# Kernel tuning notes

Hardware: AMD Instinct MI355X
Metric: run time of the kernel (lower is better)

The kernel has to match this reference:

```python
import jax, jax.numpy as jnp
import numpy as np

N, E, IN_DIM, OUT_DIM, SEM_DIM = 50000, 800000, 128, 128, 128
EPS = 1e-8


def setup_inputs() -> dict:
    key = jax.random.key(0)
    k = jax.random.split(key, 8)
    x = jax.random.normal(k[0], (N, IN_DIM), dtype=jnp.float32)
    edge_index = jax.random.randint(k[1], (2, E), 0, N, dtype=jnp.int64)
    semantic_vec = jax.random.normal(k[2], (N, SEM_DIM), dtype=jnp.float32)
    s = 1.0 / np.sqrt(IN_DIM)
    W_src = jax.random.uniform(k[3], (OUT_DIM, IN_DIM), jnp.float32, -s, s)
    b_src = jax.random.uniform(k[4], (OUT_DIM,), jnp.float32, -s, s)
    W_dst = jax.random.uniform(k[5], (OUT_DIM, IN_DIM), jnp.float32, -s, s)
    b_dst = jax.random.uniform(k[6], (OUT_DIM,), jnp.float32, -s, s)
    return {"x": x, "edge_index": edge_index, "semantic_vec": semantic_vec,
            "W_src": W_src, "b_src": b_src, "W_dst": W_dst, "b_dst": b_dst}


def _scatter_softmax(sim, dst, num_segments):
    # numerically stable segment-wise softmax over edges grouped by dst
    seg_max = jax.ops.segment_max(sim, dst, num_segments=num_segments)
    seg_max = jnp.where(jnp.isneginf(seg_max), 0.0, seg_max)
    e = jnp.exp(sim - seg_max[dst])
    seg_sum = jax.ops.segment_sum(e, dst, num_segments=num_segments)
    return e / (seg_sum[dst] + 1e-16)


def reference(x, edge_index, semantic_vec, W_src, b_src, W_dst, b_dst):
    src, dst = edge_index[0], edge_index[1]
    x_j = x[src] @ W_src.T + b_src           # [E, out_dim]
    # cosine similarity with torch eps semantics
    a = semantic_vec[src]
    b = semantic_vec[dst]
    na = jnp.maximum(jnp.linalg.norm(a, axis=-1), EPS)
    nb = jnp.maximum(jnp.linalg.norm(b, axis=-1), EPS)
    sim = jnp.sum(a * b, axis=-1) / (na * nb)  # [E]
    attn = _scatter_softmax(sim, dst, x.shape[0])
    msg = attn[:, None] * x_j                 # [E, out_dim]
    out = jax.ops.segment_sum(msg, dst, num_segments=x.shape[0])
    return out
```

## Files before the change

### kernel.cpp

```cpp
#include <hip/hip_runtime.h>
#include <hip/hip_fp16.h>

#define Nn 50000
#define Ee 800000
#define D  128
#define SLOT 64

#define B_GEMM 782
#define B_SLOT 3125
#define B_NORM 12500

struct h4 { __half2 lo, hi; };

typedef _Float16 f16x8 __attribute__((ext_vector_type(8)));
typedef float    f32x4 __attribute__((ext_vector_type(4)));

__global__ __launch_bounds__(256) void k_prep(const float* __restrict__ x,
                                              const float* __restrict__ W,
                                              const float* __restrict__ b,
                                              const int* __restrict__ ei,
                                              const float* __restrict__ sem,
                                              __half* __restrict__ y16,
                                              __half* __restrict__ sem16,
                                              int* __restrict__ cnt,
                                              int* __restrict__ slotS) {
  __shared__ __half sW[128 * 136] __attribute__((aligned(16)));
  int bid = blockIdx.x, tid = threadIdx.x;

  if (bid < B_GEMM) {
    for (int i = tid; i < 128 * 32; i += 256) {
      int r = i >> 5, c4 = (i & 31) << 2;
      float4 w = *(const float4*)(W + (size_t)r * 128 + c4);
      __half2* dst = (__half2*)&sW[r * 136 + c4];
      dst[0] = __floats2half2_rn(w.x, w.y);
      dst[1] = __floats2half2_rn(w.z, w.w);
    }
    __syncthreads();

    int wave = tid >> 6, lane = tid & 63;
    int g = lane >> 4;
    int n16 = lane & 15;
    int m0 = bid * 64 + wave * 16;
    int mA = m0 + n16; if (mA > Nn - 1) mA = Nn - 1;
    const float4* xr = (const float4*)(x + (size_t)mA * 128);

    f32x4 acc[8];
#pragma unroll
    for (int jt = 0; jt < 8; jt++) {
      float bias = b[jt * 16 + n16];
      acc[jt] = (f32x4){bias, bias, bias, bias};
    }

#pragma unroll
    for (int kt = 0; kt < 4; kt++) {
      float4 xa = xr[kt * 8 + g * 2];
      float4 xb = xr[kt * 8 + g * 2 + 1];
      f16x8 a;
      a[0] = (_Float16)xa.x; a[1] = (_Float16)xa.y; a[2] = (_Float16)xa.z; a[3] = (_Float16)xa.w;
      a[4] = (_Float16)xb.x; a[5] = (_Float16)xb.y; a[6] = (_Float16)xb.z; a[7] = (_Float16)xb.w;
#pragma unroll
      for (int jt = 0; jt < 8; jt++) {
        f16x8 bf = *(const f16x8*)(&sW[(jt * 16 + n16) * 136 + kt * 32 + g * 8]);
        acc[jt] = __builtin_amdgcn_mfma_f32_16x16x32_f16(a, bf, acc[jt], 0, 0, 0);
      }
    }

#pragma unroll
    for (int jt = 0; jt < 8; jt++) {
#pragma unroll
      for (int r = 0; r < 4; r++) {
        int row = m0 + g * 4 + r;
        if (row < Nn)
          y16[(size_t)row * 128 + jt * 16 + n16] = __float2half(acc[jt][r]);
      }
    }
  } else if (bid < B_GEMM + B_SLOT) {
    int e = (bid - B_GEMM) * 256 + tid;
    if (e < Ee) {
      int s = ei[e], d = ei[Ee + e];
      int pos = atomicAdd(cnt + d, 1);
      if (pos < SLOT)
        slotS[(size_t)d * SLOT + pos] = s;
    }
  } else {
    int n = ((bid - B_GEMM - B_SLOT) * 256 + tid) >> 6;
    int lane = tid & 63;
    if (n < Nn) {
      const float2 v = *(const float2*)(sem + (size_t)n * D + 2 * lane);
      float p = v.x * v.x + v.y * v.y;
#pragma unroll
      for (int off = 32; off > 0; off >>= 1) p += __shfl_xor(p, off);
      float inv = 1.0f / fmaxf(sqrtf(p), 1e-8f);
      *(__half2*)(sem16 + (size_t)n * D + 2 * lane) = __floats2half2_rn(v.x * inv, v.y * inv);
    }
  }
}

__global__ __launch_bounds__(256) void k_fused(const __half* __restrict__ sem16,
                                               const __half* __restrict__ y16,
                                               const int* __restrict__ slotS,
                                               const int* __restrict__ cnt,
                                               float* __restrict__ out) {
  int d = (blockIdx.x * 256 + threadIdx.x) >> 6;
  int lane = threadIdx.x & 63;
  if (d >= Nn) return;
  int sub = lane >> 5, l32 = lane & 31;
  int c = cnt[d]; if (c > SLOT) c = SLOT;

  int sv = 0;
  if (lane < c) sv = slotS[(size_t)d * SLOT + lane];

  h4 dref = ((const h4*)(sem16 + (size_t)d * D))[l32];
  float2 d0 = __half22float2(dref.lo), d1 = __half22float2(dref.hi);

  float ev = 0.0f;
  for (int i = 0; i < c; i += 4) {
    int ia = i + sub, ib = i + 2 + sub;
    int sa = __shfl(sv, ia < c ? ia : c - 1);
    int sb = __shfl(sv, ib < c ? ib : c - 1);
    h4 ra = ((const h4*)(sem16 + (size_t)sa * D))[l32];
    h4 rb = ((const h4*)(sem16 + (size_t)sb * D))[l32];
    float2 ra0 = __half22float2(ra.lo), ra1 = __half22float2(ra.hi);
    float2 rb0 = __half22float2(rb.lo), rb1 = __half22float2(rb.hi);
    float pa = d0.x * ra0.x + d0.y * ra0.y + d1.x * ra1.x + d1.y * ra1.y;
    float pb = d0.x * rb0.x + d0.y * rb0.y + d1.x * rb1.x + d1.y * rb1.y;
#pragma unroll
    for (int o = 16; o > 0; o >>= 1) { pa += __shfl_xor(pa, o); pb += __shfl_xor(pb, o); }
    float ea = expf(pa), eb = expf(pb);
    float va = __shfl(ea, (lane - i) << 5);
    float vb = __shfl(eb, (lane - i - 2) << 5);
    if (lane >= i     && lane < i + 2 && lane < c) ev = va;
    if (lane >= i + 2 && lane < i + 4 && lane < c) ev = vb;
  }

  float S = ev;
#pragma unroll
  for (int o = 32; o > 0; o >>= 1) S += __shfl_xor(S, o);
  float inv = 1.0f / (S + 1e-16f);

  float o0 = 0, o1 = 0, o2 = 0, o3 = 0;
  for (int i = 0; i < c; i += 4) {
    int ia = i + sub, ib = i + 2 + sub;
    int ca = ia < c ? ia : c - 1, cb = ib < c ? ib : c - 1;
    int sa = __shfl(sv, ca), sb = __shfl(sv, cb);
    float wa_r = __shfl(ev, ca), wb_r = __shfl(ev, cb);
    float wa = (ia < c) ? wa_r : 0.0f;
    float wb = (ib < c) ? wb_r : 0.0f;
    h4 ya = ((const h4*)(y16 + (size_t)sa * D))[l32];
    h4 yb = ((const h4*)(y16 + (size_t)sb * D))[l32];
    float2 ya0 = __half22float2(ya.lo), ya1 = __half22float2(ya.hi);
    float2 yb0 = __half22float2(yb.lo), yb1 = __half22float2(yb.hi);
    o0 += wa * ya0.x + wb * yb0.x;
    o1 += wa * ya0.y + wb * yb0.y;
    o2 += wa * ya1.x + wb * yb1.x;
    o3 += wa * ya1.y + wb * yb1.y;
  }
  o0 += __shfl_xor(o0, 32); o1 += __shfl_xor(o1, 32);
  o2 += __shfl_xor(o2, 32); o3 += __shfl_xor(o3, 32);
  if (sub == 0) {
    float4 r; r.x = o0 * inv; r.y = o1 * inv; r.z = o2 * inv; r.w = o3 * inv;
    *(float4*)(out + (size_t)d * D + l32 * 4) = r;
  }
}

extern "C" void kernel_launch(void* const* d_in, const int* in_sizes, int n_in,
                              void* d_out, int out_size, void* d_ws, size_t ws_size,
                              hipStream_t stream) {
  const float* x     = (const float*)d_in[0];
  const int*   ei    = (const int*)d_in[1];
  const float* sem   = (const float*)d_in[2];
  const float* W_src = (const float*)d_in[3];
  const float* b_src = (const float*)d_in[4];
  float* out = (float*)d_out;

  char* ws = (char*)d_ws;
  const size_t O_Y    = 0;
  const size_t O_S16  = 12800000;
  const size_t O_CNT  = 25600000;
  const size_t O_SS   = 25800000;
  const size_t NEED   = 38600000;
  if (ws_size < NEED) return;

  __half* y16   = (__half*)(ws + O_Y);
  __half* sem16 = (__half*)(ws + O_S16);
  int* cnt   = (int*)(ws + O_CNT);
  int* slotS = (int*)(ws + O_SS);

  hipMemsetAsync(cnt, 0, Nn * sizeof(int), stream);
  k_prep<<<B_GEMM + B_SLOT + B_NORM, 256, 0, stream>>>(x, W_src, b_src, ei, sem,
                                                       y16, sem16, cnt, slotS);
  k_fused<<<(Nn + 3) / 4, 256, 0, stream>>>(sem16, y16, slotS, cnt, out);
}
```

Before: 228.5 us.

## Widen per-iteration gathers, use fdot2, drop LDS weight staging, coarsen prep blocks

The fused kernel now handles four neighbors per half-wave per iteration instead of two, computes the cosine dot with packed fp16 dot instructions, and stores exp values in shared memory instead of shuffling them. Normalization is folded into the weights before aggregation. In the prep kernel, the GEMM reads W directly from global/L2 and converts it in registers instead of staging fp16 W in LDS, and the scatter and norm blocks each process more items per thread. These aim to raise memory-level parallelism and cut block and LDS overhead, at the cost of redundant W loads per wave and more register pressure.

```diff
diff --git a/kernel.cpp b/kernel.cpp
--- a/kernel.cpp
+++ b/kernel.cpp
@@ -7,13 +7,30 @@
 #define SLOT 64
 
 #define B_GEMM 782
-#define B_SLOT 3125
-#define B_NORM 12500
+#define B_SCAT 1563
+#define B_NORM 3125
 
 struct h4 { __half2 lo, hi; };
 
 typedef _Float16 f16x8 __attribute__((ext_vector_type(8)));
+typedef _Float16 f16x2 __attribute__((ext_vector_type(2)));
 typedef float    f32x4 __attribute__((ext_vector_type(4)));
+
+union H2 { __half2 h; f16x2 v; };
+
+__device__ __forceinline__ float dot4(h4 a, h4 b, float acc) {
+#if __has_builtin(__builtin_amdgcn_fdot2)
+  H2 al, ah, bl, bh;
+  al.h = a.lo; ah.h = a.hi; bl.h = b.lo; bh.h = b.hi;
+  acc = __builtin_amdgcn_fdot2(al.v, bl.v, acc, false);
+  acc = __builtin_amdgcn_fdot2(ah.v, bh.v, acc, false);
+  return acc;
+#else
+  float2 a0 = __half22float2(a.lo), a1 = __half22float2(a.hi);
+  float2 b0 = __half22float2(b.lo), b1 = __half22float2(b.hi);
+  return acc + a0.x * b0.x + a0.y * b0.y + a1.x * b1.x + a1.y * b1.y;
+#endif
+}
 
 __global__ __launch_bounds__(256) void k_prep(const float* __restrict__ x,
                                               const float* __restrict__ W,
@@ -24,19 +41,9 @@
                                               __half* __restrict__ sem16,
                                               int* __restrict__ cnt,
                                               int* __restrict__ slotS) {
-  __shared__ __half sW[128 * 136] __attribute__((aligned(16)));
   int bid = blockIdx.x, tid = threadIdx.x;
 
   if (bid < B_GEMM) {
-    for (int i = tid; i < 128 * 32; i += 256) {
-      int r = i >> 5, c4 = (i & 31) << 2;
-      float4 w = *(const float4*)(W + (size_t)r * 128 + c4);
-      __half2* dst = (__half2*)&sW[r * 136 + c4];
-      dst[0] = __floats2half2_rn(w.x, w.y);
-      dst[1] = __floats2half2_rn(w.z, w.w);
-    }
-    __syncthreads();
-
     int wave = tid >> 6, lane = tid & 63;
     int g = lane >> 4;
     int n16 = lane & 15;
@@ -60,7 +67,11 @@
       a[4] = (_Float16)xb.x; a[5] = (_Float16)xb.y; a[6] = (_Float16)xb.z; a[7] = (_Float16)xb.w;
 #pragma unroll
       for (int jt = 0; jt < 8; jt++) {
-        f16x8 bf = *(const f16x8*)(&sW[(jt * 16 + n16) * 136 + kt * 32 + g * 8]);
+        const float4* wr = (const float4*)(W + (size_t)(jt * 16 + n16) * 128 + kt * 32 + g * 8);
+        float4 w0 = wr[0], w1 = wr[1];
+        f16x8 bf;
+        bf[0] = (_Float16)w0.x; bf[1] = (_Float16)w0.y; bf[2] = (_Float16)w0.z; bf[3] = (_Float16)w0.w;
+        bf[4] = (_Float16)w1.x; bf[5] = (_Float16)w1.y; bf[6] = (_Float16)w1.z; bf[7] = (_Float16)w1.w;
         acc[jt] = __builtin_amdgcn_mfma_f32_16x16x32_f16(a, bf, acc[jt], 0, 0, 0);
       }
     }
@@ -74,18 +85,24 @@
           y16[(size_t)row * 128 + jt * 16 + n16] = __float2half(acc[jt][r]);
       }
     }
-  } else if (bid < B_GEMM + B_SLOT) {
-    int e = (bid - B_GEMM) * 256 + tid;
-    if (e < Ee) {
-      int s = ei[e], d = ei[Ee + e];
-      int pos = atomicAdd(cnt + d, 1);
-      if (pos < SLOT)
-        slotS[(size_t)d * SLOT + pos] = s;
+  } else if (bid < B_GEMM + B_SCAT) {
+    int base = (bid - B_GEMM) * 512 + tid;
+#pragma unroll
+    for (int u = 0; u < 2; u++) {
+      int e = base + u * 256;
+      if (e < Ee) {
+        int s = ei[e], d = ei[Ee + e];
+        int pos = atomicAdd(cnt + d, 1);
+        if (pos < SLOT)
+          slotS[(size_t)d * SLOT + pos] = s;
+      }
     }
   } else {
-    int n = ((bid - B_GEMM - B_SLOT) * 256 + tid) >> 6;
-    int lane = tid & 63;
-    if (n < Nn) {
+    int nb = (bid - B_GEMM - B_SCAT) * 16;
+    int wave = tid >> 6, lane = tid & 63;
+#pragma unroll
+    for (int it = 0; it < 4; it++) {
+      int n = nb + it * 4 + wave;
       const float2 v = *(const float2*)(sem + (size_t)n * D + 2 * lane);
       float p = v.x * v.x + v.y * v.y;
 #pragma unroll
@@ -101,64 +118,79 @@
                                                const int* __restrict__ slotS,
                                                const int* __restrict__ cnt,
                                                float* __restrict__ out) {
-  int d = (blockIdx.x * 256 + threadIdx.x) >> 6;
-  int lane = threadIdx.x & 63;
+  __shared__ float sev[4][SLOT];
+  int w = threadIdx.x >> 6, lane = threadIdx.x & 63;
+  int d = blockIdx.x * 4 + w;
   if (d >= Nn) return;
   int sub = lane >> 5, l32 = lane & 31;
   int c = cnt[d]; if (c > SLOT) c = SLOT;
 
-  int sv = 0;
-  if (lane < c) sv = slotS[(size_t)d * SLOT + lane];
+  int sv = (lane < c) ? slotS[(size_t)d * SLOT + lane] : 0;
 
   h4 dref = ((const h4*)(sem16 + (size_t)d * D))[l32];
-  float2 d0 = __half22float2(dref.lo), d1 = __half22float2(dref.hi);
-
-  float ev = 0.0f;
-  for (int i = 0; i < c; i += 4) {
-    int ia = i + sub, ib = i + 2 + sub;
-    int sa = __shfl(sv, ia < c ? ia : c - 1);
-    int sb = __shfl(sv, ib < c ? ib : c - 1);
-    h4 ra = ((const h4*)(sem16 + (size_t)sa * D))[l32];
-    h4 rb = ((const h4*)(sem16 + (size_t)sb * D))[l32];
-    float2 ra0 = __half22float2(ra.lo), ra1 = __half22float2(ra.hi);
-    float2 rb0 = __half22float2(rb.lo), rb1 = __half22float2(rb.hi);
-    float pa = d0.x * ra0.x + d0.y * ra0.y + d1.x * ra1.x + d1.y * ra1.y;
-    float pb = d0.x * rb0.x + d0.y * rb0.y + d1.x * rb1.x + d1.y * rb1.y;
-#pragma unroll
-    for (int o = 16; o > 0; o >>= 1) { pa += __shfl_xor(pa, o); pb += __shfl_xor(pb, o); }
-    float ea = expf(pa), eb = expf(pb);
-    float va = __shfl(ea, (lane - i) << 5);
-    float vb = __shfl(eb, (lane - i - 2) << 5);
-    if (lane >= i     && lane < i + 2 && lane < c) ev = va;
-    if (lane >= i + 2 && lane < i + 4 && lane < c) ev = vb;
-  }
-
+
+  for (int i = 0; i < c; i += 8) {
+    float p0 = 0, p1 = 0, p2 = 0, p3 = 0;
+    int i0 = i + sub * 4;
+    int c0 = min(i0,     c - 1), c1 = min(i0 + 1, c - 1);
+    int c2 = min(i0 + 2, c - 1), c3 = min(i0 + 3, c - 1);
+    int s0 = __shfl(sv, c0), s1 = __shfl(sv, c1);
+    int s2 = __shfl(sv, c2), s3 = __shfl(sv, c3);
+    h4 r0 = ((const h4*)(sem16 + (size_t)s0 * D))[l32];
+    h4 r1 = ((const h4*)(sem16 + (size_t)s1 * D))[l32];
+    h4 r2 = ((const h4*)(sem16 + (size_t)s2 * D))[l32];
+    h4 r3 = ((const h4*)(sem16 + (size_t)s3 * D))[l32];
+    p0 = dot4(dref, r0, p0); p1 = dot4(dref, r1, p1);
+    p2 = dot4(dref, r2, p2); p3 = dot4(dref, r3, p3);
+#pragma unroll
+    for (int o = 16; o > 0; o >>= 1) {
+      p0 += __shfl_xor(p0, o); p1 += __shfl_xor(p1, o);
+      p2 += __shfl_xor(p2, o); p3 += __shfl_xor(p3, o);
+    }
+    float pe = p0;
+    pe = (l32 == 1) ? p1 : pe;
+    pe = (l32 == 2) ? p2 : pe;
+    pe = (l32 == 3) ? p3 : pe;
+    int iu = i0 + l32;
+    if (l32 < 4 && iu < c) sev[w][iu] = __expf(pe);
+  }
+
+  float ev = (lane < c) ? sev[w][lane] : 0.0f;
   float S = ev;
 #pragma unroll
   for (int o = 32; o > 0; o >>= 1) S += __shfl_xor(S, o);
-  float inv = 1.0f / (S + 1e-16f);
+  float evs = ev / (S + 1e-16f);
 
   float o0 = 0, o1 = 0, o2 = 0, o3 = 0;
-  for (int i = 0; i < c; i += 4) {
-    int ia = i + sub, ib = i + 2 + sub;
-    int ca = ia < c ? ia : c - 1, cb = ib < c ? ib : c - 1;
-    int sa = __shfl(sv, ca), sb = __shfl(sv, cb);
-    float wa_r = __shfl(ev, ca), wb_r = __shfl(ev, cb);
-    float wa = (ia < c) ? wa_r : 0.0f;
-    float wb = (ib < c) ? wb_r : 0.0f;
-    h4 ya = ((const h4*)(y16 + (size_t)sa * D))[l32];
-    h4 yb = ((const h4*)(y16 + (size_t)sb * D))[l32];
-    float2 ya0 = __half22float2(ya.lo), ya1 = __half22float2(ya.hi);
-    float2 yb0 = __half22float2(yb.lo), yb1 = __half22float2(yb.hi);
-    o0 += wa * ya0.x + wb * yb0.x;
-    o1 += wa * ya0.y + wb * yb0.y;
-    o2 += wa * ya1.x + wb * yb1.x;
-    o3 += wa * ya1.y + wb * yb1.y;
+  for (int i = 0; i < c; i += 8) {
+    int i0 = i + sub * 4;
+    int c0 = min(i0,     c - 1), c1 = min(i0 + 1, c - 1);
+    int c2 = min(i0 + 2, c - 1), c3 = min(i0 + 3, c - 1);
+    int s0 = __shfl(sv, c0), s1 = __shfl(sv, c1);
+    int s2 = __shfl(sv, c2), s3 = __shfl(sv, c3);
+    float w0 = __shfl(evs, c0), w1 = __shfl(evs, c1);
+    float w2 = __shfl(evs, c2), w3 = __shfl(evs, c3);
+    if (i0     >= c) w0 = 0;
+    if (i0 + 1 >= c) w1 = 0;
+    if (i0 + 2 >= c) w2 = 0;
+    if (i0 + 3 >= c) w3 = 0;
+    h4 ya = ((const h4*)(y16 + (size_t)s0 * D))[l32];
+    h4 yb = ((const h4*)(y16 + (size_t)s1 * D))[l32];
+    h4 yc = ((const h4*)(y16 + (size_t)s2 * D))[l32];
+    h4 yd = ((const h4*)(y16 + (size_t)s3 * D))[l32];
+    float2 a0 = __half22float2(ya.lo), a1 = __half22float2(ya.hi);
+    float2 b0 = __half22float2(yb.lo), b1 = __half22float2(yb.hi);
+    float2 e0 = __half22float2(yc.lo), e1 = __half22float2(yc.hi);
+    float2 f0 = __half22float2(yd.lo), f1 = __half22float2(yd.hi);
+    o0 += w0 * a0.x + w1 * b0.x + w2 * e0.x + w3 * f0.x;
+    o1 += w0 * a0.y + w1 * b0.y + w2 * e0.y + w3 * f0.y;
+    o2 += w0 * a1.x + w1 * b1.x + w2 * e1.x + w3 * f1.x;
+    o3 += w0 * a1.y + w1 * b1.y + w2 * e1.y + w3 * f1.y;
   }
   o0 += __shfl_xor(o0, 32); o1 += __shfl_xor(o1, 32);
   o2 += __shfl_xor(o2, 32); o3 += __shfl_xor(o3, 32);
   if (sub == 0) {
-    float4 r; r.x = o0 * inv; r.y = o1 * inv; r.z = o2 * inv; r.w = o3 * inv;
+    float4 r; r.x = o0; r.y = o1; r.z = o2; r.w = o3;
     *(float4*)(out + (size_t)d * D + l32 * 4) = r;
   }
 }
@@ -187,7 +219,7 @@
   int* slotS = (int*)(ws + O_SS);
 
   hipMemsetAsync(cnt, 0, Nn * sizeof(int), stream);
-  k_prep<<<B_GEMM + B_SLOT + B_NORM, 256, 0, stream>>>(x, W_src, b_src, ei, sem,
+  k_prep<<<B_GEMM + B_SCAT + B_NORM, 256, 0, stream>>>(x, W_src, b_src, ei, sem,
                                                        y16, sem16, cnt, slotS);
   k_fused<<<(Nn + 3) / 4, 256, 0, stream>>>(sem16, y16, slotS, cnt, out);
 }
```

Measured after the change: 241.5 us. 5.7% more time.

## Pad degree counters, drop LDS weight staging, use fdot2 and fast exp

Applied to the files above, without the earlier changes.

Several independent tweaks. Per-node atomic counters are padded to a 64-byte stride to reduce atomic contention on shared cache lines. The GEMM branch now reads W straight from global memory and converts it per MFMA instead of staging it in LDS. Scatter and normalize blocks each process more items per thread. The fused kernel uses the fdot2 intrinsic for the half-precision dot products and __expf instead of expf. In exchange, the counter memset grows 16x and W is reloaded from global/cache many times, which adds traffic and conversion work in the GEMM.

```diff
diff --git a/kernel.cpp b/kernel.cpp
--- a/kernel.cpp
+++ b/kernel.cpp
@@ -5,15 +5,32 @@
 #define Ee 800000
 #define D  128
 #define SLOT 64
+#define CSTR 16
 
 #define B_GEMM 782
-#define B_SLOT 3125
-#define B_NORM 12500
+#define B_SCAT 1563
+#define B_NORM 3125
 
 struct h4 { __half2 lo, hi; };
 
 typedef _Float16 f16x8 __attribute__((ext_vector_type(8)));
+typedef _Float16 f16x2 __attribute__((ext_vector_type(2)));
 typedef float    f32x4 __attribute__((ext_vector_type(4)));
+
+union H2 { __half2 h; f16x2 v; };
+
+__device__ __forceinline__ float dot4(h4 a, h4 b) {
+#if __has_builtin(__builtin_amdgcn_fdot2)
+  H2 al, ah, bl, bh;
+  al.h = a.lo; ah.h = a.hi; bl.h = b.lo; bh.h = b.hi;
+  float acc = __builtin_amdgcn_fdot2(al.v, bl.v, 0.0f, false);
+  return __builtin_amdgcn_fdot2(ah.v, bh.v, acc, false);
+#else
+  float2 a0 = __half22float2(a.lo), a1 = __half22float2(a.hi);
+  float2 b0 = __half22float2(b.lo), b1 = __half22float2(b.hi);
+  return a0.x * b0.x + a0.y * b0.y + a1.x * b1.x + a1.y * b1.y;
+#endif
+}
 
 __global__ __launch_bounds__(256) void k_prep(const float* __restrict__ x,
                                               const float* __restrict__ W,
@@ -24,19 +41,9 @@
                                               __half* __restrict__ sem16,
                                               int* __restrict__ cnt,
                                               int* __restrict__ slotS) {
-  __shared__ __half sW[128 * 136] __attribute__((aligned(16)));
   int bid = blockIdx.x, tid = threadIdx.x;
 
   if (bid < B_GEMM) {
-    for (int i = tid; i < 128 * 32; i += 256) {
-      int r = i >> 5, c4 = (i & 31) << 2;
-      float4 w = *(const float4*)(W + (size_t)r * 128 + c4);
-      __half2* dst = (__half2*)&sW[r * 136 + c4];
-      dst[0] = __floats2half2_rn(w.x, w.y);
-      dst[1] = __floats2half2_rn(w.z, w.w);
-    }
-    __syncthreads();
-
     int wave = tid >> 6, lane = tid & 63;
     int g = lane >> 4;
     int n16 = lane & 15;
@@ -60,7 +67,11 @@
       a[4] = (_Float16)xb.x; a[5] = (_Float16)xb.y; a[6] = (_Float16)xb.z; a[7] = (_Float16)xb.w;
 #pragma unroll
       for (int jt = 0; jt < 8; jt++) {
-        f16x8 bf = *(const f16x8*)(&sW[(jt * 16 + n16) * 136 + kt * 32 + g * 8]);
+        const float4* wr = (const float4*)(W + (size_t)(jt * 16 + n16) * 128 + kt * 32 + g * 8);
+        float4 w0 = wr[0], w1 = wr[1];
+        f16x8 bf;
+        bf[0] = (_Float16)w0.x; bf[1] = (_Float16)w0.y; bf[2] = (_Float16)w0.z; bf[3] = (_Float16)w0.w;
+        bf[4] = (_Float16)w1.x; bf[5] = (_Float16)w1.y; bf[6] = (_Float16)w1.z; bf[7] = (_Float16)w1.w;
         acc[jt] = __builtin_amdgcn_mfma_f32_16x16x32_f16(a, bf, acc[jt], 0, 0, 0);
       }
     }
@@ -74,18 +85,24 @@
           y16[(size_t)row * 128 + jt * 16 + n16] = __float2half(acc[jt][r]);
       }
     }
-  } else if (bid < B_GEMM + B_SLOT) {
-    int e = (bid - B_GEMM) * 256 + tid;
-    if (e < Ee) {
-      int s = ei[e], d = ei[Ee + e];
-      int pos = atomicAdd(cnt + d, 1);
-      if (pos < SLOT)
-        slotS[(size_t)d * SLOT + pos] = s;
+  } else if (bid < B_GEMM + B_SCAT) {
+    int base = (bid - B_GEMM) * 512 + tid;
+#pragma unroll
+    for (int u = 0; u < 2; u++) {
+      int e = base + u * 256;
+      if (e < Ee) {
+        int s = ei[e], d = ei[Ee + e];
+        int pos = atomicAdd(cnt + (size_t)d * CSTR, 1);
+        if (pos < SLOT)
+          slotS[(size_t)d * SLOT + pos] = s;
+      }
     }
   } else {
-    int n = ((bid - B_GEMM - B_SLOT) * 256 + tid) >> 6;
-    int lane = tid & 63;
-    if (n < Nn) {
+    int nb = (bid - B_GEMM - B_SCAT) * 16;
+    int wave = tid >> 6, lane = tid & 63;
+#pragma unroll
+    for (int it = 0; it < 4; it++) {
+      int n = nb + it * 4 + wave;
       const float2 v = *(const float2*)(sem + (size_t)n * D + 2 * lane);
       float p = v.x * v.x + v.y * v.y;
 #pragma unroll
@@ -105,13 +122,11 @@
   int lane = threadIdx.x & 63;
   if (d >= Nn) return;
   int sub = lane >> 5, l32 = lane & 31;
-  int c = cnt[d]; if (c > SLOT) c = SLOT;
-
-  int sv = 0;
-  if (lane < c) sv = slotS[(size_t)d * SLOT + lane];
+  int c = cnt[(size_t)d * CSTR]; if (c > SLOT) c = SLOT;
+
+  int sv = (lane < c) ? slotS[(size_t)d * SLOT + lane] : 0;
 
   h4 dref = ((const h4*)(sem16 + (size_t)d * D))[l32];
-  float2 d0 = __half22float2(dref.lo), d1 = __half22float2(dref.hi);
 
   float ev = 0.0f;
   for (int i = 0; i < c; i += 4) {
@@ -120,13 +135,11 @@
     int sb = __shfl(sv, ib < c ? ib : c - 1);
     h4 ra = ((const h4*)(sem16 + (size_t)sa * D))[l32];
     h4 rb = ((const h4*)(sem16 + (size_t)sb * D))[l32];
-    float2 ra0 = __half22float2(ra.lo), ra1 = __half22float2(ra.hi);
-    float2 rb0 = __half22float2(rb.lo), rb1 = __half22float2(rb.hi);
-    float pa = d0.x * ra0.x + d0.y * ra0.y + d1.x * ra1.x + d1.y * ra1.y;
-    float pb = d0.x * rb0.x + d0.y * rb0.y + d1.x * rb1.x + d1.y * rb1.y;
+    float pa = dot4(dref, ra);
+    float pb = dot4(dref, rb);
 #pragma unroll
     for (int o = 16; o > 0; o >>= 1) { pa += __shfl_xor(pa, o); pb += __shfl_xor(pb, o); }
-    float ea = expf(pa), eb = expf(pb);
+    float ea = __expf(pa), eb = __expf(pb);
     float va = __shfl(ea, (lane - i) << 5);
     float vb = __shfl(eb, (lane - i - 2) << 5);
     if (lane >= i     && lane < i + 2 && lane < c) ev = va;
@@ -148,12 +161,12 @@
     float wb = (ib < c) ? wb_r : 0.0f;
     h4 ya = ((const h4*)(y16 + (size_t)sa * D))[l32];
     h4 yb = ((const h4*)(y16 + (size_t)sb * D))[l32];
-    float2 ya0 = __half22float2(ya.lo), ya1 = __half22float2(ya.hi);
-    float2 yb0 = __half22float2(yb.lo), yb1 = __half22float2(yb.hi);
-    o0 += wa * ya0.x + wb * yb0.x;
-    o1 += wa * ya0.y + wb * yb0.y;
-    o2 += wa * ya1.x + wb * yb1.x;
-    o3 += wa * ya1.y + wb * yb1.y;
+    float2 a0 = __half22float2(ya.lo), a1 = __half22float2(ya.hi);
+    float2 b0 = __half22float2(yb.lo), b1 = __half22float2(yb.hi);
+    o0 += wa * a0.x + wb * b0.x;
+    o1 += wa * a0.y + wb * b0.y;
+    o2 += wa * a1.x + wb * b1.x;
+    o3 += wa * a1.y + wb * b1.y;
   }
   o0 += __shfl_xor(o0, 32); o1 += __shfl_xor(o1, 32);
   o2 += __shfl_xor(o2, 32); o3 += __shfl_xor(o3, 32);
@@ -177,8 +190,8 @@
   const size_t O_Y    = 0;
   const size_t O_S16  = 12800000;
   const size_t O_CNT  = 25600000;
-  const size_t O_SS   = 25800000;
-  const size_t NEED   = 38600000;
+  const size_t O_SS   = 28800000;
+  const size_t NEED   = 41600000;
   if (ws_size < NEED) return;
 
   __half* y16   = (__half*)(ws + O_Y);
@@ -186,8 +199,8 @@
   int* cnt   = (int*)(ws + O_CNT);
   int* slotS = (int*)(ws + O_SS);
 
-  hipMemsetAsync(cnt, 0, Nn * sizeof(int), stream);
-  k_prep<<<B_GEMM + B_SLOT + B_NORM, 256, 0, stream>>>(x, W_src, b_src, ei, sem,
+  hipMemsetAsync(cnt, 0, (size_t)Nn * CSTR * sizeof(int), stream);
+  k_prep<<<B_GEMM + B_SCAT + B_NORM, 256, 0, stream>>>(x, W_src, b_src, ei, sem,
                                                        y16, sem16, cnt, slotS);
   k_fused<<<(Nn + 3) / 4, 256, 0, stream>>>(sem16, y16, slotS, cnt, out);
 }
```

Result: faster. 223.3 us (-2.3%).
